# Performance work log

Measured on AMD Instinct MI355X. Metric: run time of the kernel, lower is better.

Reference implementation:

```python
import jax, jax.numpy as jnp
import numpy as np

B, N, D, T = 32, 512, 128, 8
NEG_SLOPE = 0.2
MASK_VAL = -1e10


def _xavier(key, shape, gain=1.0):
    fan_in, fan_out = shape[0], int(np.prod(shape[1:]))
    limit = gain * np.sqrt(6.0 / (fan_in + fan_out))
    return jax.random.uniform(key, shape, jnp.float32, -limit, limit)


def setup_inputs() -> dict:
    key = jax.random.key(0)
    ks = jax.random.split(key, 8)
    atom_embeddings = jax.random.normal(ks[0], (B, N, D), dtype=jnp.float32)
    # bond types in [-1, T-1]; -1 = no bond (masked)
    edges = jax.random.randint(ks[1], (B, N, N), 0, T + 1, dtype=jnp.int64) - 1
    Qw = _xavier(ks[2], (D, D))
    Kw = _xavier(ks[3], (D, D))
    Vw = _xavier(ks[4], (D, D))
    Pw = _xavier(ks[5], (D, D))
    Qb = jnp.zeros((D,), jnp.float32)
    Kb = jnp.zeros((D,), jnp.float32)
    Vb = jnp.zeros((D,), jnp.float32)
    Pb = jnp.zeros((D,), jnp.float32)
    a = _xavier(ks[6], (D, D, T), gain=1.414)
    return {"atom_embeddings": atom_embeddings, "edges": edges,
            "Qw": Qw, "Qb": Qb, "Kw": Kw, "Kb": Kb, "Vw": Vw, "Vb": Vb,
            "a": a, "Pw": Pw, "Pb": Pb}


def reference(atom_embeddings, edges, Qw, Qb, Kw, Kb, Vw, Vb, a, Pw, Pb):
    # torch Linear: x @ W.T + b
    src = atom_embeddings @ Qw.T + Qb            # (B,N,D)
    dst = atom_embeddings @ Kw.T + Kb            # (B,N,D)
    val = atom_embeddings @ Vw.T + Vb            # (B,N,D)

    # bilinear edge-type scores: s[b,n,m,t] = src[b,n,:] @ a[:,:,t] @ dst[b,m,:]
    ts = jnp.einsum('bnd,det->bnet', src, a)     # (B,N,D,T)
    scores = jnp.einsum('bnet,bme->bnmt', ts, dst)  # (B,N,N,T)

    # gather the slice for each edge's bond type (clamp -1 -> 0 like torch)
    idx = jnp.clip(edges, 0, None)[..., None]    # (B,N,N,1)
    att = jnp.take_along_axis(scores, idx, axis=-1)[..., 0]  # (B,N,N)
    att = jnp.where(edges == -1, MASK_VAL, att)
    att = jnp.where(att >= 0, att, NEG_SLOPE * att)  # leaky_relu
    att = jax.nn.softmax(att, axis=-1)           # (B,N,N)

    out = att @ val                              # (B,N,D)
    return out @ Pw.T + Pb
```

## Files before the change

kernel.cpp:

```cpp
#include <hip/hip_runtime.h>
#include <stdint.h>


typedef short bf16x8 __attribute__((ext_vector_type(8)));
typedef float f32x4 __attribute__((ext_vector_type(4)));
typedef unsigned short u16;
typedef unsigned int u32;
typedef unsigned long long u64;

__device__ __forceinline__ u16 f2bf(float x) {
    union { float f; u32 u; } v; v.f = x;
    u32 r = v.u + 0x7FFFu + ((v.u >> 16) & 1u);
    return (u16)(r >> 16);
}
__device__ __forceinline__ float bf2f(u16 h) {
    union { u32 u; float f; } v; v.u = ((u32)h) << 16; return v.f;
}
__device__ __forceinline__ void split_hl(float x, u16& h, u16& l) {
    h = f2bf(x);
    l = f2bf(x - bf2f(h));
}
__device__ __forceinline__ void split4(float4 x, u64& hq, u64& lq) {
    u16 h0, l0, h1, l1, h2, l2, h3, l3;
    split_hl(x.x, h0, l0); split_hl(x.y, h1, l1);
    split_hl(x.z, h2, l2); split_hl(x.w, h3, l3);
    hq = (u64)h0 | ((u64)h1 << 16) | ((u64)h2 << 32) | ((u64)h3 << 48);
    lq = (u64)l0 | ((u64)l1 << 16) | ((u64)l2 << 32) | ((u64)l3 << 48);
}
__device__ __forceinline__ void split8(float4 a, float4 b, bf16x8& h8, bf16x8& l8) {
    u16 hh[8], ll[8];
    split_hl(a.x, hh[0], ll[0]); split_hl(a.y, hh[1], ll[1]);
    split_hl(a.z, hh[2], ll[2]); split_hl(a.w, hh[3], ll[3]);
    split_hl(b.x, hh[4], ll[4]); split_hl(b.y, hh[5], ll[5]);
    split_hl(b.z, hh[6], ll[6]); split_hl(b.w, hh[7], ll[7]);
    #pragma unroll
    for (int i = 0; i < 8; i++) { h8[i] = (short)hh[i]; l8[i] = (short)ll[i]; }
}
__device__ __forceinline__ f32x4 mfma16(bf16x8 a, bf16x8 b, f32x4 c) {
    return __builtin_amdgcn_mfma_f32_16x16x32_bf16(a, b, c, 0, 0, 0);
}

__global__ void prep_kernel(const float* __restrict__ Qw, const float* __restrict__ Qb,
                            const float* __restrict__ Kw, const float* __restrict__ Kb,
                            const float* __restrict__ Vw, const float* __restrict__ Vb,
                            const float* __restrict__ Aa, const float* __restrict__ Pw,
                            u16* __restrict__ WFH, u16* __restrict__ WFL,
                            float* __restrict__ bcat) {
    int gid = blockIdx.x * 256 + threadIdx.x;
    if (gid >= 1280 * 128) return;
    int j = gid >> 7, d = gid & 127;
    float v, bias = 0.f;
    if (j < 128) { v = Kw[j * 128 + d]; bias = Kb[j]; }
    else if (j < 256) {
        int jj = j - 128;
        float s = 0.f, bs = 0.f;
        for (int k = 0; k < 128; k++) {
            float p = Pw[jj * 128 + k];
            s += p * Vw[k * 128 + d];
            bs += p * Vb[k];
        }
        v = s; bias = bs;
    } else {
        int r = j - 256, t = r >> 7, jj = r & 127;
        float s = 0.f, bs = 0.f;
        for (int e = 0; e < 128; e++) {
            float av = Aa[(e * 128 + jj) * 8 + t];
            s += Qw[e * 128 + d] * av;
            bs += Qb[e] * av;
        }
        v = s; bias = bs;
    }
    u16 h, l; split_hl(v, h, l);
    size_t idx = ((size_t)((j >> 4) * 16 + (d >> 3)) * 16 + (j & 15)) * 8 + (d & 7);
    WFH[idx] = h; WFL[idx] = l;
    if (d == 0) bcat[j] = bias;
}

__global__ void detect_kernel(const int* __restrict__ E, int* __restrict__ flag) {
    __shared__ int bad;
    if (threadIdx.x == 0) bad = 0;
    __syncthreads();
    int w0 = E[2 * threadIdx.x + 1];
    int w1 = E[2 * (threadIdx.x + 256) + 1];
    if (!(w0 == 0 || w0 == -1) || !(w1 == 0 || w1 == -1)) atomicOr(&bad, 1);
    __syncthreads();
    if (threadIdx.x == 0) *flag = (bad ? 0 : 1);
}

__launch_bounds__(256, 3)
__global__ void gemm1_kernel(const float* __restrict__ X,
                             const u16* __restrict__ WFH, const u16* __restrict__ WFL,
                             const float* __restrict__ bcat,
                             u16* __restrict__ FSH, u16* __restrict__ FSL,
                             u16* __restrict__ FBH, u16* __restrict__ FBL,
                             u16* __restrict__ VTH, u16* __restrict__ VTL) {
    const int id = blockIdx.x;
    const int xcd = id & 7, q = id >> 3;
    const int g0 = (xcd * 32 + (q >> 2)) * 64;
    const int jsplit = q & 3;
    const int tid = threadIdx.x;
    const int wid = tid >> 6, lane = tid & 63;
    const int gblk = (wid >> 1) * 32, jblk = (wid & 1) * 32;
    const int lr = lane & 15, lg = lane >> 4;

    bf16x8 afh[4][2], afl[4][2];
    #pragma unroll
    for (int ks = 0; ks < 4; ks++)
    #pragma unroll
    for (int r = 0; r < 2; r++) {
        const float* p = X + (size_t)(g0 + gblk + r * 16 + lr) * 128 + ks * 32 + lg * 8;
        float4 a = *(const float4*)p;
        float4 b = *(const float4*)(p + 4);
        split8(a, b, afh[ks][r], afl[ks][r]);
    }
    const int b = g0 >> 9;

    #pragma unroll
    for (int jt5 = 0; jt5 < 5; jt5++) {
        const int jt = jsplit * 5 + jt5;
        const int j0 = jt * 64;
        const bool valTile = (jt == 2 || jt == 3);
        const int jgbase = (j0 + jblk) >> 4;
        f32x4 acc[2][2] = {};
        if (valTile) {
            #pragma unroll
            for (int ks = 0; ks < 4; ks++) {
                bf16x8 bfh[2], bfl[2];
                #pragma unroll
                for (int c = 0; c < 2; c++) {
                    size_t eo = ((size_t)((jgbase + c) * 16 + ks * 4 + lg) * 16 + lr) * 8;
                    bfh[c] = *(const bf16x8*)(WFH + eo);
                    bfl[c] = *(const bf16x8*)(WFL + eo);
                }
                #pragma unroll
                for (int r = 0; r < 2; r++)
                #pragma unroll
                for (int c = 0; c < 2; c++) {
                    acc[r][c] = mfma16(afh[ks][r], bfh[c], acc[r][c]);
                    acc[r][c] = mfma16(afh[ks][r], bfl[c], acc[r][c]);
                    acc[r][c] = mfma16(afl[ks][r], bfh[c], acc[r][c]);
                }
            }
            #pragma unroll
            for (int r = 0; r < 2; r++)
            #pragma unroll
            for (int c = 0; c < 2; c++) {
                int j = j0 + jblk + c * 16 + lr;
                float bias = bcat[j];
                int d = j - 128;
                int n = (g0 & 511) + gblk + r * 16 + 4 * lg;
                float4 v = {acc[r][c][0] + bias, acc[r][c][1] + bias,
                            acc[r][c][2] + bias, acc[r][c][3] + bias};
                u64 hq, lq; split4(v, hq, lq);
                size_t off = ((size_t)(b * 128 + d)) * 512 + n;
                *(u64*)(VTH + off) = hq;
                *(u64*)(VTL + off) = lq;
            }
        } else {
            #pragma unroll
            for (int ks = 0; ks < 4; ks++) {
                bf16x8 bfh[2], bfl[2];
                #pragma unroll
                for (int c = 0; c < 2; c++) {
                    size_t eo = ((size_t)((jgbase + c) * 16 + ks * 4 + lg) * 16 + lr) * 8;
                    bfh[c] = *(const bf16x8*)(WFH + eo);
                    bfl[c] = *(const bf16x8*)(WFL + eo);
                }
                #pragma unroll
                for (int c = 0; c < 2; c++)
                #pragma unroll
                for (int r = 0; r < 2; r++) {
                    acc[c][r] = mfma16(bfh[c], afh[ks][r], acc[c][r]);
                    acc[c][r] = mfma16(bfh[c], afl[ks][r], acc[c][r]);
                    acc[c][r] = mfma16(bfl[c], afh[ks][r], acc[c][r]);
                }
            }
            if (jt < 2) {
                const int mt = (g0 & 511) >> 7;
                const int mbase = g0 & 127;
                size_t fb = (size_t)(b * 4 + mt) * 16384;
                #pragma unroll
                for (int c = 0; c < 2; c++)
                #pragma unroll
                for (int r = 0; r < 2; r++) {
                    int d0 = j0 + jblk + c * 16 + 4 * lg;
                    float4 bias4 = *(const float4*)(bcat + d0);
                    float4 v = {acc[c][r][0] + bias4.x, acc[c][r][1] + bias4.y,
                                acc[c][r][2] + bias4.z, acc[c][r][3] + bias4.w};
                    u64 hq, lq; split4(v, hq, lq);
                    int kc = (d0 >> 5) * 4 + ((d0 >> 3) & 3);
                    int mrow = mbase + gblk + r * 16 + lr;
                    size_t off = fb + ((size_t)kc * 128 + mrow) * 8 + (d0 & 7);
                    *(u64*)(FBH + off) = hq;
                    *(u64*)(FBL + off) = lq;
                }
            } else {
                const int nt = (g0 & 511) >> 6;
                const int tt = (jt - 4) >> 1;
                size_t fs = ((size_t)(b * 8 + nt) * 8 + tt) * 8192;
                #pragma unroll
                for (int c = 0; c < 2; c++)
                #pragma unroll
                for (int r = 0; r < 2; r++) {
                    int j = j0 + jblk + c * 16 + 4 * lg;
                    float4 bias4 = *(const float4*)(bcat + j);
                    float4 v = {acc[c][r][0] + bias4.x, acc[c][r][1] + bias4.y,
                                acc[c][r][2] + bias4.z, acc[c][r][3] + bias4.w};
                    u64 hq, lq; split4(v, hq, lq);
                    int d0 = ((jt - 4) & 1) * 64 + jblk + c * 16 + 4 * lg;
                    int kc = (d0 >> 5) * 4 + ((d0 >> 3) & 3);
                    int nrow = gblk + r * 16 + lr;
                    size_t off = fs + ((size_t)kc * 64 + nrow) * 8 + (d0 & 7);
                    *(u64*)(FSH + off) = hq;
                    *(u64*)(FSL + off) = lq;
                }
            }
        }
    }
}

__launch_bounds__(256, 3)
__global__ void scores_kernel(const u16* __restrict__ FSH, const u16* __restrict__ FSL,
                              const u16* __restrict__ FBH, const u16* __restrict__ FBL,
                              const void* __restrict__ Eptr, const int* __restrict__ flag,
                              float* __restrict__ att) {
    const int id = blockIdx.x;
    const int xcd = id & 7, s = id >> 3;
    const int b = xcd * 4 + (s >> 6);
    const int tile = s & 63;
    const int n0 = (tile >> 3) * 64, m0 = (tile & 7) * 64;
    const int nt = n0 >> 6;
    const int mt = m0 >> 7, mb = m0 & 127;
    const int tid = threadIdx.x;
    const int wid = tid >> 6, lane = tid & 63;
    const int wr = (wid >> 1) * 32, wc = (wid & 1) * 32;
    const int lr = lane & 15, lg = lane >> 4;
    const bool e64 = (*flag != 0);

    int ed[2][2][4];
    #pragma unroll
    for (int r = 0; r < 2; r++)
    #pragma unroll
    for (int c = 0; c < 2; c++)
    #pragma unroll
    for (int q = 0; q < 4; q++) {
        size_t n = n0 + wr + r * 16 + 4 * lg + q;
        size_t m = m0 + wc + c * 16 + lr;
        size_t idx = ((size_t)b * 512 + n) * 512 + m;
        ed[r][c][q] = e64 ? (int)((const long long*)Eptr)[idx] : ((const int*)Eptr)[idx];
    }
    bf16x8 bfh[4][2], bfl[4][2];
    #pragma unroll
    for (int ks = 0; ks < 4; ks++)
    #pragma unroll
    for (int c = 0; c < 2; c++) {
        size_t eo = (size_t)(b * 4 + mt) * 16384
                  + ((size_t)((ks * 4 + lg) * 128 + mb + wc + c * 16 + lr)) * 8;
        bfh[ks][c] = *(const bf16x8*)(FBH + eo);
        bfl[ks][c] = *(const bf16x8*)(FBL + eo);
    }
    float sel[2][2][4];
    #pragma unroll
    for (int r = 0; r < 2; r++)
    #pragma unroll
    for (int c = 0; c < 2; c++)
    #pragma unroll
    for (int q = 0; q < 4; q++) sel[r][c][q] = 0.f;

    const size_t abase0 = (size_t)(b * 8 + nt) * 8 * 8192;
    #pragma unroll 1
    for (int t = 0; t < 8; t++) {
        const size_t abase = abase0 + (size_t)t * 8192;
        f32x4 acc[2][2] = {};
        #pragma unroll
        for (int ks = 0; ks < 4; ks++) {
            bf16x8 afh[2], afl[2];
            #pragma unroll
            for (int r = 0; r < 2; r++) {
                size_t eo = abase + ((size_t)((ks * 4 + lg) * 64 + wr + r * 16 + lr)) * 8;
                afh[r] = *(const bf16x8*)(FSH + eo);
                afl[r] = *(const bf16x8*)(FSL + eo);
            }
            #pragma unroll
            for (int r = 0; r < 2; r++)
            #pragma unroll
            for (int c = 0; c < 2; c++) {
                acc[r][c] = mfma16(afh[r], bfh[ks][c], acc[r][c]);
                acc[r][c] = mfma16(afh[r], bfl[ks][c], acc[r][c]);
                acc[r][c] = mfma16(afl[r], bfh[ks][c], acc[r][c]);
            }
        }
        #pragma unroll
        for (int r = 0; r < 2; r++)
        #pragma unroll
        for (int c = 0; c < 2; c++)
        #pragma unroll
        for (int q = 0; q < 4; q++) {
            int ec = ed[r][c][q] < 0 ? 0 : ed[r][c][q];
            sel[r][c][q] = (ec == t) ? acc[r][c][q] : sel[r][c][q];
        }
    }
    #pragma unroll
    for (int r = 0; r < 2; r++)
    #pragma unroll
    for (int c = 0; c < 2; c++)
    #pragma unroll
    for (int q = 0; q < 4; q++) {
        float v = (ed[r][c][q] == -1) ? -1e10f : sel[r][c][q];
        v = (v >= 0.f) ? v : 0.2f * v;
        size_t n = n0 + wr + r * 16 + 4 * lg + q;
        size_t m = m0 + wc + c * 16 + lr;
        att[((size_t)b * 512 + n) * 512 + m] = v;
    }
}

__launch_bounds__(256, 2)
__global__ void out_kernel(const float* __restrict__ att,
                           const u16* __restrict__ VTH, const u16* __restrict__ VTL,
                           const float* __restrict__ Pb, float* __restrict__ out) {
    const int id = blockIdx.x;
    const int xcd = id & 7, j = id >> 3;
    const int b = xcd * 4 + (j >> 4);
    const int n0 = (j & 15) * 32;
    __shared__ u16 PH[32 * 64], PL[32 * 64];
    __shared__ u16 VH[128 * 64], VL[128 * 64];
    const int tid = threadIdx.x;
    const int row = tid >> 3, c8 = tid & 7;
    float4 av0[8], av1[8];
    const float4* rp = (const float4*)(att + ((size_t)b * 512 + n0 + row) * 512);
    #pragma unroll
    for (int mc = 0; mc < 8; mc++) {
        av0[mc] = rp[mc * 16 + c8 * 2];
        av1[mc] = rp[mc * 16 + c8 * 2 + 1];
    }
    float mx = -1e30f;
    #pragma unroll
    for (int mc = 0; mc < 8; mc++) {
        mx = fmaxf(mx, fmaxf(fmaxf(fmaxf(av0[mc].x, av0[mc].y), fmaxf(av0[mc].z, av0[mc].w)),
                             fmaxf(fmaxf(av1[mc].x, av1[mc].y), fmaxf(av1[mc].z, av1[mc].w))));
    }
    #pragma unroll
    for (int o = 1; o < 8; o <<= 1) mx = fmaxf(mx, __shfl_xor(mx, o, 64));
    float s = 0.f;
    #pragma unroll
    for (int mc = 0; mc < 8; mc++) {
        av0[mc].x = expf(av0[mc].x - mx); av0[mc].y = expf(av0[mc].y - mx);
        av0[mc].z = expf(av0[mc].z - mx); av0[mc].w = expf(av0[mc].w - mx);
        av1[mc].x = expf(av1[mc].x - mx); av1[mc].y = expf(av1[mc].y - mx);
        av1[mc].z = expf(av1[mc].z - mx); av1[mc].w = expf(av1[mc].w - mx);
        s += av0[mc].x + av0[mc].y + av0[mc].z + av0[mc].w
           + av1[mc].x + av1[mc].y + av1[mc].z + av1[mc].w;
    }
    #pragma unroll
    for (int o = 1; o < 8; o <<= 1) s += __shfl_xor(s, o, 64);
    const float inv = 1.0f / s;
    const int wid = tid >> 6, lane = tid & 63;
    const int lr = lane & 15, lg = lane >> 4;
    const int wc = wid * 32;
    f32x4 acc[2][2] = {};
    for (int mc = 0; mc < 8; mc++) {
        {
            float4 p0 = {av0[mc].x * inv, av0[mc].y * inv, av0[mc].z * inv, av0[mc].w * inv};
            float4 p1 = {av1[mc].x * inv, av1[mc].y * inv, av1[mc].z * inv, av1[mc].w * inv};
            u64 h0, l0, h1, l1;
            split4(p0, h0, l0); split4(p1, h1, l1);
            int boff = (row * 128 + c8 * 16) ^ ((row & 7) << 4);
            *(u64*)((char*)PH + boff) = h0;
            *(u64*)((char*)PH + boff + 8) = h1;
            *(u64*)((char*)PL + boff) = l0;
            *(u64*)((char*)PL + boff + 8) = l1;
        }
        #pragma unroll
        for (int i = 0; i < 4; i++) {
            int idx = tid + i * 256;
            int vrow = idx >> 3, ch = idx & 7;
            size_t src = ((size_t)(b * 128 + vrow)) * 512 + mc * 64;
            int boff = (vrow * 128 + ch * 16) ^ ((vrow & 7) << 4);
            *(uint4*)((char*)VH + boff) = ((const uint4*)(VTH + src))[ch];
            *(uint4*)((char*)VL + boff) = ((const uint4*)(VTL + src))[ch];
        }
        __syncthreads();
        #pragma unroll
        for (int ks = 0; ks < 2; ks++) {
            const int kb2 = (ks * 32 + lg * 8) * 2;
            bf16x8 ah[2], al[2];
            #pragma unroll
            for (int r = 0; r < 2; r++) {
                int prow = r * 16 + lr;
                int boff = (prow * 128 + kb2) ^ ((prow & 7) << 4);
                ah[r] = *(const bf16x8*)((const char*)PH + boff);
                al[r] = *(const bf16x8*)((const char*)PL + boff);
            }
            #pragma unroll
            for (int c = 0; c < 2; c++) {
                int vrow = wc + c * 16 + lr;
                int boff = (vrow * 128 + kb2) ^ ((vrow & 7) << 4);
                bf16x8 bh = *(const bf16x8*)((const char*)VH + boff);
                bf16x8 bl = *(const bf16x8*)((const char*)VL + boff);
                #pragma unroll
                for (int r = 0; r < 2; r++) {
                    acc[r][c] = mfma16(ah[r], bh, acc[r][c]);
                    acc[r][c] = mfma16(ah[r], bl, acc[r][c]);
                    acc[r][c] = mfma16(al[r], bh, acc[r][c]);
                }
            }
        }
        __syncthreads();
    }
    #pragma unroll
    for (int r = 0; r < 2; r++)
    #pragma unroll
    for (int c = 0; c < 2; c++)
    #pragma unroll
    for (int q = 0; q < 4; q++) {
        int n = n0 + r * 16 + 4 * lg + q;
        int d = wc + c * 16 + lr;
        out[((size_t)b * 512 + n) * 128 + d] = acc[r][c][q] + Pb[d];
    }
}

extern "C" void kernel_launch(void* const* d_in, const int* in_sizes, int n_in,
                              void* d_out, int out_size, void* d_ws, size_t ws_size,
                              hipStream_t stream) {
    (void)in_sizes; (void)n_in; (void)out_size; (void)ws_size;
    const float* X  = (const float*)d_in[0];
    const void*  E  = d_in[1];
    const float* Qw = (const float*)d_in[2];
    const float* Qb = (const float*)d_in[3];
    const float* Kw = (const float*)d_in[4];
    const float* Kb = (const float*)d_in[5];
    const float* Vw = (const float*)d_in[6];
    const float* Vb = (const float*)d_in[7];
    const float* Aa = (const float*)d_in[8];
    const float* Pw = (const float*)d_in[9];
    const float* Pb = (const float*)d_in[10];
    float* out = (float*)d_out;

    char* ws = (char*)d_ws;
    size_t cur = 0;
    auto alloc = [&](size_t bytes) -> char* {
        char* p = ws + cur;
        cur += (bytes + 255) & ~(size_t)255;
        return p;
    };
    int*   flag = (int*)  alloc(4);
    u16*   WFH  = (u16*)  alloc((size_t)1280 * 128 * 2);
    u16*   WFL  = (u16*)  alloc((size_t)1280 * 128 * 2);
    float* bcat = (float*)alloc(1280 * 4);
    u16*   FSH  = (u16*)  alloc((size_t)32 * 8 * 8 * 8192 * 2);
    u16*   FSL  = (u16*)  alloc((size_t)32 * 8 * 8 * 8192 * 2);
    u16*   FBH  = (u16*)  alloc((size_t)32 * 4 * 16384 * 2);
    u16*   FBL  = (u16*)  alloc((size_t)32 * 4 * 16384 * 2);
    u16*   VTH  = (u16*)  alloc((size_t)32 * 128 * 512 * 2);
    u16*   VTL  = (u16*)  alloc((size_t)32 * 128 * 512 * 2);
    float* att  = (float*)alloc((size_t)32 * 512 * 512 * 4);

    prep_kernel<<<640, 256, 0, stream>>>(Qw, Qb, Kw, Kb, Vw, Vb, Aa, Pw, WFH, WFL, bcat);
    detect_kernel<<<1, 256, 0, stream>>>((const int*)E, flag);
    gemm1_kernel<<<1024, 256, 0, stream>>>(X, WFH, WFL, bcat, FSH, FSL, FBH, FBL, VTH, VTL);
    scores_kernel<<<2048, 256, 0, stream>>>(FSH, FSL, FBH, FBL, E, flag, att);
    out_kernel<<<512, 256, 0, stream>>>(att, VTH, VTL, Pb, out);
}
```

Measured before the change: 242.7 us.

## Enlarge scores kernel tiles to 128x128 with 64x64 per-wave register blocking

```diff
diff --git a/kernel.cpp b/kernel.cpp
--- a/kernel.cpp
+++ b/kernel.cpp
@@ -87,7 +87,7 @@
     if (threadIdx.x == 0) *flag = (bad ? 0 : 1);
 }
 
-__launch_bounds__(256, 3)
+__launch_bounds__(256, 4)
 __global__ void gemm1_kernel(const float* __restrict__ X,
                              const u16* __restrict__ WFH, const u16* __restrict__ WFL,
                              const float* __restrict__ bcat,
@@ -219,97 +219,106 @@
     }
 }
 
-__launch_bounds__(256, 3)
+__launch_bounds__(256, 2)
 __global__ void scores_kernel(const u16* __restrict__ FSH, const u16* __restrict__ FSL,
                               const u16* __restrict__ FBH, const u16* __restrict__ FBL,
                               const void* __restrict__ Eptr, const int* __restrict__ flag,
                               float* __restrict__ att) {
     const int id = blockIdx.x;
-    const int xcd = id & 7, s = id >> 3;
-    const int b = xcd * 4 + (s >> 6);
-    const int tile = s & 63;
-    const int n0 = (tile >> 3) * 64, m0 = (tile & 7) * 64;
-    const int nt = n0 >> 6;
-    const int mt = m0 >> 7, mb = m0 & 127;
+    const int xcd = id & 7, r5 = id >> 3;
+    const int b = xcd * 4 + (r5 >> 4);
+    const int tile = r5 & 15;
+    const int n0 = (tile >> 2) * 128, m0 = (tile & 3) * 128;
     const int tid = threadIdx.x;
     const int wid = tid >> 6, lane = tid & 63;
-    const int wr = (wid >> 1) * 32, wc = (wid & 1) * 32;
+    const int wn = n0 + (wid >> 1) * 64, wm = m0 + (wid & 1) * 64;
     const int lr = lane & 15, lg = lane >> 4;
     const bool e64 = (*flag != 0);
-
-    int ed[2][2][4];
-    #pragma unroll
-    for (int r = 0; r < 2; r++)
-    #pragma unroll
-    for (int c = 0; c < 2; c++)
-    #pragma unroll
-    for (int q = 0; q < 4; q++) {
-        size_t n = n0 + wr + r * 16 + 4 * lg + q;
-        size_t m = m0 + wc + c * 16 + lr;
-        size_t idx = ((size_t)b * 512 + n) * 512 + m;
-        ed[r][c][q] = e64 ? (int)((const long long*)Eptr)[idx] : ((const int*)Eptr)[idx];
-    }
-    bf16x8 bfh[4][2], bfl[4][2];
-    #pragma unroll
-    for (int ks = 0; ks < 4; ks++)
-    #pragma unroll
-    for (int c = 0; c < 2; c++) {
-        size_t eo = (size_t)(b * 4 + mt) * 16384
-                  + ((size_t)((ks * 4 + lg) * 128 + mb + wc + c * 16 + lr)) * 8;
-        bfh[ks][c] = *(const bf16x8*)(FBH + eo);
-        bfl[ks][c] = *(const bf16x8*)(FBL + eo);
-    }
-    float sel[2][2][4];
-    #pragma unroll
-    for (int r = 0; r < 2; r++)
-    #pragma unroll
-    for (int c = 0; c < 2; c++)
+    const int estride = e64 ? 2 : 1;
+
+    u32 edpk[4][4];
+    u64 mneg = 0;
+    #pragma unroll
+    for (int r = 0; r < 4; r++)
+    #pragma unroll
+    for (int c = 0; c < 4; c++) {
+        u32 pk = 0;
+        #pragma unroll
+        for (int q = 0; q < 4; q++) {
+            size_t n = wn + r * 16 + 4 * lg + q;
+            size_t m = wm + c * 16 + lr;
+            size_t idx = ((size_t)b * 512 + n) * 512 + m;
+            int e = ((const int*)Eptr)[idx * estride];
+            pk |= (u32)(e & 0xff) << (q * 8);
+            if (e < 0) mneg |= 1ull << (r * 16 + c * 4 + q);
+        }
+        edpk[r][c] = pk;
+    }
+
+    const size_t abase0 = ((size_t)(b * 8 + (wn >> 6)) * 8) * 8192
+                        + (size_t)(lg * 64 + lr) * 8;
+    const size_t bbase0 = (size_t)(b * 4 + (wm >> 7)) * 16384
+                        + (size_t)(lg * 128 + (wm & 127) + lr) * 8;
+
+    float sel[4][4][4];
+    #pragma unroll
+    for (int r = 0; r < 4; r++)
+    #pragma unroll
+    for (int c = 0; c < 4; c++)
     #pragma unroll
     for (int q = 0; q < 4; q++) sel[r][c][q] = 0.f;
 
-    const size_t abase0 = (size_t)(b * 8 + nt) * 8 * 8192;
     #pragma unroll 1
     for (int t = 0; t < 8; t++) {
+        f32x4 acc[4][4] = {};
         const size_t abase = abase0 + (size_t)t * 8192;
-        f32x4 acc[2][2] = {};
         #pragma unroll
         for (int ks = 0; ks < 4; ks++) {
-            bf16x8 afh[2], afl[2];
-            #pragma unroll
-            for (int r = 0; r < 2; r++) {
-                size_t eo = abase + ((size_t)((ks * 4 + lg) * 64 + wr + r * 16 + lr)) * 8;
+            bf16x8 afh[4], afl[4], bfh[4], bfl[4];
+            #pragma unroll
+            for (int r = 0; r < 4; r++) {
+                size_t eo = abase + (size_t)(ks * 4 * 64 + r * 16) * 8;
                 afh[r] = *(const bf16x8*)(FSH + eo);
                 afl[r] = *(const bf16x8*)(FSL + eo);
             }
             #pragma unroll
-            for (int r = 0; r < 2; r++)
-            #pragma unroll
-            for (int c = 0; c < 2; c++) {
-                acc[r][c] = mfma16(afh[r], bfh[ks][c], acc[r][c]);
-                acc[r][c] = mfma16(afh[r], bfl[ks][c], acc[r][c]);
-                acc[r][c] = mfma16(afl[r], bfh[ks][c], acc[r][c]);
-            }
-        }
-        #pragma unroll
-        for (int r = 0; r < 2; r++)
-        #pragma unroll
-        for (int c = 0; c < 2; c++)
-        #pragma unroll
-        for (int q = 0; q < 4; q++) {
-            int ec = ed[r][c][q] < 0 ? 0 : ed[r][c][q];
-            sel[r][c][q] = (ec == t) ? acc[r][c][q] : sel[r][c][q];
-        }
-    }
-    #pragma unroll
-    for (int r = 0; r < 2; r++)
-    #pragma unroll
-    for (int c = 0; c < 2; c++)
+            for (int c = 0; c < 4; c++) {
+                size_t eo = bbase0 + (size_t)(ks * 4 * 128 + c * 16) * 8;
+                bfh[c] = *(const bf16x8*)(FBH + eo);
+                bfl[c] = *(const bf16x8*)(FBL + eo);
+            }
+            #pragma unroll
+            for (int r = 0; r < 4; r++)
+            #pragma unroll
+            for (int c = 0; c < 4; c++) {
+                acc[r][c] = mfma16(afh[r], bfh[c], acc[r][c]);
+                acc[r][c] = mfma16(afh[r], bfl[c], acc[r][c]);
+                acc[r][c] = mfma16(afl[r], bfh[c], acc[r][c]);
+            }
+        }
+        #pragma unroll
+        for (int r = 0; r < 4; r++)
+        #pragma unroll
+        for (int c = 0; c < 4; c++) {
+            u32 x = edpk[r][c];
+            #pragma unroll
+            for (int q = 0; q < 4; q++) {
+                bool hit = ((x >> (q * 8)) & 0xffu) == (u32)t;
+                sel[r][c][q] = hit ? acc[r][c][q] : sel[r][c][q];
+            }
+        }
+    }
+    #pragma unroll
+    for (int r = 0; r < 4; r++)
+    #pragma unroll
+    for (int c = 0; c < 4; c++)
     #pragma unroll
     for (int q = 0; q < 4; q++) {
-        float v = (ed[r][c][q] == -1) ? -1e10f : sel[r][c][q];
+        bool neg = (mneg >> (r * 16 + c * 4 + q)) & 1;
+        float v = neg ? -1e10f : sel[r][c][q];
         v = (v >= 0.f) ? v : 0.2f * v;
-        size_t n = n0 + wr + r * 16 + 4 * lg + q;
-        size_t m = m0 + wc + c * 16 + lr;
+        size_t n = wn + r * 16 + 4 * lg + q;
+        size_t m = wm + c * 16 + lr;
         att[((size_t)b * 512 + n) * 512 + m] = v;
     }
 }
@@ -458,6 +467,6 @@
     prep_kernel<<<640, 256, 0, stream>>>(Qw, Qb, Kw, Kb, Vw, Vb, Aa, Pw, WFH, WFL, bcat);
     detect_kernel<<<1, 256, 0, stream>>>((const int*)E, flag);
     gemm1_kernel<<<1024, 256, 0, stream>>>(X, WFH, WFL, bcat, FSH, FSL, FBH, FBL, VTH, VTL);
-    scores_kernel<<<2048, 256, 0, stream>>>(FSH, FSL, FBH, FBL, E, flag, att);
+    scores_kernel<<<512, 256, 0, stream>>>(FSH, FSL, FBH, FBL, E, flag, att);
     out_kernel<<<512, 256, 0, stream>>>(att, VTH, VTL, Pb, out);
 }
```

New measurement: 408.9 us. 1.68x slower.
